# Kernel tuning notes

Hardware: AMD Instinct MI355X
Metric: run time of the kernel (lower is better)

Reference implementation:

```python
import jax, jax.numpy as jnp
import numpy as np

BETA = 0.25
N_E = 1024
E_DIM = 64
B, L = 32, 2048


def setup_inputs() -> dict:
    key = jax.random.key(0)
    k1, k2 = jax.random.split(key)
    z = jax.random.normal(k1, (B, L, E_DIM), dtype=jnp.float32)
    # torch init: uniform_(-1/n_e, 1/n_e)
    codebook = jax.random.uniform(k2, (N_E, E_DIM), dtype=jnp.float32,
                                  minval=-1.0 / N_E, maxval=1.0 / N_E)
    return {"z": z, "codebook": codebook}


def reference(z, codebook):
    sg = jax.lax.stop_gradient
    n_e = codebook.shape[0]
    zf = z.reshape(-1, codebook.shape[1])  # (N, e_dim)
    # squared-distance matrix: ||z||^2 + ||e||^2 - 2 z.e  -> (N, n_e)
    d = (jnp.sum(zf * zf, axis=1, keepdims=True)
         + jnp.sum(codebook * codebook, axis=1)
         - 2.0 * zf @ codebook.T)
    idx = jnp.argmin(d, axis=1)  # (N,)
    # one-hot @ codebook is just a gather
    z_q = codebook[idx].reshape(z.shape)
    loss = (jnp.mean((sg(z_q) - z) ** 2)
            + BETA * jnp.mean((z_q - sg(z)) ** 2))
    # straight-through estimator
    z_q_st = z + sg(z_q - z)
    # codebook usage stats (mean of one-hot rows == normalized histogram)
    counts = jnp.zeros((n_e,), dtype=z.dtype).at[idx].add(1.0)
    e_mean = counts / idx.shape[0]
    perplexity = jnp.exp(-jnp.sum(e_mean * jnp.log(e_mean + 1e-10)))
    return loss, z_q_st, perplexity, idx
```

## Files before the change

kernel.cpp:

```cpp
#include <hip/hip_runtime.h>
#include <math.h>

#define E_DIM 64
#define N_E   1024
#define BETA  0.25

using bf16x8 = __attribute__((ext_vector_type(8))) short;
using f32x4  = __attribute__((ext_vector_type(4))) float;
#define MFMA(a, b, c) __builtin_amdgcn_mfma_f32_16x16x32_bf16((a), (b), (c), 0, 0, 0)


__device__ __forceinline__ unsigned short f2bf_rn(float f) {
    unsigned u = __builtin_bit_cast(unsigned, f);
    unsigned r = u + 0x7fffu + ((u >> 16) & 1u);
    return (unsigned short)(r >> 16);
}
__device__ __forceinline__ float bf2f(unsigned short b) {
    unsigned u = ((unsigned)b) << 16;
    return __builtin_bit_cast(float, u);
}

__device__ __forceinline__ float pw64_sq(const float* v) {
    float r[8];
#pragma unroll
    for (int l = 0; l < 8; ++l) r[l] = v[l] * v[l];
#pragma unroll
    for (int t = 1; t < 8; ++t)
#pragma unroll
        for (int l = 0; l < 8; ++l) r[l] += v[8 * t + l] * v[8 * t + l];
    return ((r[0] + r[1]) + (r[2] + r[3])) + ((r[4] + r[5]) + (r[6] + r[7]));
}

__global__ __launch_bounds__(256) void k_prep(const float* __restrict__ cb,
                                              unsigned short* __restrict__ ebh,
                                              unsigned short* __restrict__ ebl,
                                              float* __restrict__ h,
                                              unsigned* __restrict__ hist,
                                              double* __restrict__ sse,
                                              unsigned* __restrict__ flagN) {
    int t = blockIdx.x * 256 + threadIdx.x;
    {
        int e = t & 7, lane = (t >> 3) & 63, ks = (t >> 9) & 1, ct = t >> 10;
        int j = ct * 16 + (lane & 15);
        int k = ks * 32 + ((lane >> 4) << 3) + e;
        float v = cb[j * 64 + k];
        unsigned short hi = f2bf_rn(v);
        ebh[t] = hi;
        ebl[t] = f2bf_rn(v - bf2f(hi));
    }
    if (blockIdx.x < 4) {
        int j = t;
        float e[E_DIM];
        const float4* ep = reinterpret_cast<const float4*>(cb + (size_t)j * E_DIM);
#pragma unroll
        for (int k4 = 0; k4 < E_DIM / 4; ++k4) {
            float4 v = ep[k4];
            e[4 * k4 + 0] = v.x; e[4 * k4 + 1] = v.y;
            e[4 * k4 + 2] = v.z; e[4 * k4 + 3] = v.w;
        }
        h[j] = pw64_sq(e);
    } else if (blockIdx.x == 4) {
#pragma unroll
        for (int u = 0; u < 4; ++u) hist[threadIdx.x * 4 + u] = 0u;
    } else if (blockIdx.x == 5 && threadIdx.x == 0) {
        *sse = 0.0;
        *flagN = 0u;
    }
}

__global__ __launch_bounds__(256, 2) void k_mfma(
    const float* __restrict__ z, const float* __restrict__ cb,
    const float* __restrict__ h,
    const unsigned short* __restrict__ ebh, const unsigned short* __restrict__ ebl,
    float* __restrict__ out_zq, float* __restrict__ out_idx,
    unsigned* __restrict__ hist, double* __restrict__ sse,
    unsigned* __restrict__ flagN, unsigned* __restrict__ flagL) {
    const int lane = threadIdx.x & 63;
    const int w = __builtin_amdgcn_readfirstlane(threadIdx.x >> 6);
    const int m = lane & 15, g = lane >> 4;

    __shared__ int bok;
    __shared__ float rsv[4][32];
    __shared__ float sb0[4][32], sb1[4][32];
    __shared__ int   sbi[4][32];
    if (threadIdx.x == 0) bok = 1;
    __syncthreads();

    {
        bf16x8 a, b;
#pragma unroll
        for (int e = 0; e < 8; ++e) {
            int k = g * 8 + e;
            a[e] = (short)f2bf_rn((float)(((m * 3 + k * 7) & 15) - 7));
            b[e] = (short)f2bf_rn((float)(((k * 5 + m * 3) & 15) - 8));
        }
        f32x4 acc = {0.f, 0.f, 0.f, 0.f};
        acc = MFMA(a, b, acc);
        bool ok = true;
#pragma unroll
        for (int r = 0; r < 4; ++r) {
            int rw = g * 4 + r;
            float E = 0.f;
            for (int k = 0; k < 32; ++k)
                E += (float)((((rw * 3 + k * 7) & 15) - 7) * (((k * 5 + m * 3) & 15) - 8));
            ok = ok && (acc[r] == E);
        }
        if (!ok) atomicAnd(&bok, 0);
    }
    __syncthreads();
    if (!bok) {
        if (threadIdx.x < 128) {
            unsigned p = atomicAdd(flagN, 1u);
            flagL[p] = (unsigned)(blockIdx.x * 128 + threadIdx.x);
        }
        return;
    }

    const int rowb32 = blockIdx.x * 128 + w * 32;
    bf16x8 a0h0, a0l0, a0h1, a0l1, a1h0, a1l0, a1h1, a1l1;
#define ALOAD(P, AH0, AL0, AH1, AL1) {                                         \
        const int rowA = rowb32 + (P) * 16 + m;                                \
        const float4* zr = reinterpret_cast<const float4*>(z + (size_t)rowA * 64); \
        float4 p0 = zr[g * 2], p1 = zr[g * 2 + 1];                             \
        float4 p2 = zr[8 + g * 2], p3 = zr[9 + g * 2];                         \
        float t0[8] = {p0.x, p0.y, p0.z, p0.w, p1.x, p1.y, p1.z, p1.w};        \
        float t1[8] = {p2.x, p2.y, p2.z, p2.w, p3.x, p3.y, p3.z, p3.w};        \
        float s = 0.f;                                                         \
        _Pragma("unroll")                                                      \
        for (int e = 0; e < 8; ++e) {                                          \
            s += fabsf(t0[e]) + fabsf(t1[e]);                                  \
            float x0 = 2.0f * t0[e]; unsigned short h0 = f2bf_rn(x0);          \
            AH0[e] = (short)h0; AL0[e] = (short)f2bf_rn(x0 - bf2f(h0));        \
            float x1 = 2.0f * t1[e]; unsigned short h1 = f2bf_rn(x1);          \
            AH1[e] = (short)h1; AL1[e] = (short)f2bf_rn(x1 - bf2f(h1));        \
        }                                                                      \
        s += __shfl_xor(s, 16);                                                \
        s += __shfl_xor(s, 32);                                                \
        if (g == 0) rsv[w][(P) * 16 + m] = s;                                  \
    }
    ALOAD(0, a0h0, a0l0, a0h1, a0l1)
    ALOAD(1, a1h0, a1l0, a1h1, a1l1)
#undef ALOAD

    float bb00 = INFINITY, bb01 = INFINITY, bb02 = INFINITY, bb03 = INFINITY;
    float bb10 = INFINITY, bb11 = INFINITY, bb12 = INFINITY, bb13 = INFINITY;
    float ss00 = INFINITY, ss01 = INFINITY, ss02 = INFINITY, ss03 = INFINITY;
    float ss10 = INFINITY, ss11 = INFINITY, ss12 = INFINITY, ss13 = INFINITY;
    int   ii00 = 0, ii01 = 0, ii02 = 0, ii03 = 0;
    int   ii10 = 0, ii11 = 0, ii12 = 0, ii13 = 0;
#define UPD(S, B0, B1, I0) { float _s = (S);                                   \
        if (_s < B0) { B1 = B0; B0 = _s; I0 = j; } else B1 = fminf(B1, _s); }

    const bf16x8* pBh = reinterpret_cast<const bf16x8*>(ebh);
    const bf16x8* pBl = reinterpret_cast<const bf16x8*>(ebl);

    bf16x8 Ah0 = pBh[lane],       Ah1 = pBh[lane + 64];
    bf16x8 Al0 = pBl[lane],       Al1 = pBl[lane + 64];
    bf16x8 Bh0 = pBh[128 + lane], Bh1 = pBh[128 + lane + 64];
    bf16x8 Bl0 = pBl[128 + lane], Bl1 = pBl[128 + lane + 64];

#define COLTILE(CT, VH0, VH1, VL0, VL1) {                                      \
        const int j = (CT) * 16 + m;                                           \
        const float hj = h[j];                                                 \
        const f32x4 z4 = {0.f, 0.f, 0.f, 0.f};                                 \
        f32x4 c0a = MFMA(a0h0, VH0, z4);                                       \
        f32x4 c0b = MFMA(a0h1, VH1, z4);                                       \
        f32x4 c1a = MFMA(a1h0, VH0, z4);                                       \
        f32x4 c1b = MFMA(a1h1, VH1, z4);                                       \
        f32x4 c0c = MFMA(a0h0, VL0, z4);                                       \
        f32x4 c0d = MFMA(a0h1, VL1, z4);                                       \
        f32x4 c1c = MFMA(a1h0, VL0, z4);                                       \
        f32x4 c1d = MFMA(a1h1, VL1, z4);                                       \
        f32x4 c0e = MFMA(a0l0, VH0, z4);                                       \
        f32x4 c0f = MFMA(a0l1, VH1, z4);                                       \
        f32x4 c1e = MFMA(a1l0, VH0, z4);                                       \
        f32x4 c1f = MFMA(a1l1, VH1, z4);                                       \
        f32x4 s0 = (c0a + c0b) + ((c0c + c0d) + (c0e + c0f));                  \
        f32x4 s1 = (c1a + c1b) + ((c1c + c1d) + (c1e + c1f));                  \
        UPD(hj - s0[0], bb00, ss00, ii00)                                      \
        UPD(hj - s0[1], bb01, ss01, ii01)                                      \
        UPD(hj - s0[2], bb02, ss02, ii02)                                      \
        UPD(hj - s0[3], bb03, ss03, ii03)                                      \
        UPD(hj - s1[0], bb10, ss10, ii10)                                      \
        UPD(hj - s1[1], bb11, ss11, ii11)                                      \
        UPD(hj - s1[2], bb12, ss12, ii12)                                      \
        UPD(hj - s1[3], bb13, ss13, ii13)                                      \
    }

#pragma unroll 1
    for (int ct = 0; ct < 64; ct += 2) {
        COLTILE(ct, Ah0, Ah1, Al0, Al1);
        if (ct + 2 < 64) {
            const int fb = (ct + 2) * 128 + lane;
            Ah0 = pBh[fb]; Ah1 = pBh[fb + 64];
            Al0 = pBl[fb]; Al1 = pBl[fb + 64];
        }
        COLTILE(ct + 1, Bh0, Bh1, Bl0, Bl1);
        if (ct + 3 < 64) {
            const int fb = (ct + 3) * 128 + lane;
            Bh0 = pBh[fb]; Bh1 = pBh[fb + 64];
            Bl0 = pBl[fb]; Bl1 = pBl[fb + 64];
        }
    }
#undef COLTILE
#undef UPD

#pragma unroll
    for (int mask = 1; mask < 16; mask <<= 1) {
#define MRG(B0, I0, B1) { float ob0 = __shfl_xor(B0, mask); int oi = __shfl_xor(I0, mask); \
        float ob1 = __shfl_xor(B1, mask); \
        if (ob0 < B0) { B1 = fminf(fminf(B0, B1), ob1); B0 = ob0; I0 = oi; } \
        else { B1 = fminf(B1, fminf(ob0, ob1)); } }
        MRG(bb00, ii00, ss00) MRG(bb01, ii01, ss01)
        MRG(bb02, ii02, ss02) MRG(bb03, ii03, ss03)
        MRG(bb10, ii10, ss10) MRG(bb11, ii11, ss11)
        MRG(bb12, ii12, ss12) MRG(bb13, ii13, ss13)
#undef MRG
    }

    if (m == 0) {
        sb0[w][g * 4 + 0] = bb00; sb1[w][g * 4 + 0] = ss00; sbi[w][g * 4 + 0] = ii00;
        sb0[w][g * 4 + 1] = bb01; sb1[w][g * 4 + 1] = ss01; sbi[w][g * 4 + 1] = ii01;
        sb0[w][g * 4 + 2] = bb02; sb1[w][g * 4 + 2] = ss02; sbi[w][g * 4 + 2] = ii02;
        sb0[w][g * 4 + 3] = bb03; sb1[w][g * 4 + 3] = ss03; sbi[w][g * 4 + 3] = ii03;
        sb0[w][16 + g * 4 + 0] = bb10; sb1[w][16 + g * 4 + 0] = ss10; sbi[w][16 + g * 4 + 0] = ii10;
        sb0[w][16 + g * 4 + 1] = bb11; sb1[w][16 + g * 4 + 1] = ss11; sbi[w][16 + g * 4 + 1] = ii11;
        sb0[w][16 + g * 4 + 2] = bb12; sb1[w][16 + g * 4 + 2] = ss12; sbi[w][16 + g * 4 + 2] = ii12;
        sb0[w][16 + g * 4 + 3] = bb13; sb1[w][16 + g * 4 + 3] = ss13; sbi[w][16 + g * 4 + 3] = ii13;
    }
    __syncthreads();

    {
        const int rloc = lane >> 1, q = lane & 1;
        const int rowO = rowb32 + rloc;
        const float vb0 = sb0[w][rloc];
        const float vb1 = sb1[w][rloc];
        const int   vi  = sbi[w][rloc];
        const float Delta = 6e-8f * rsv[w][rloc] + 2.2e-5f;
        float local = 0.f;
        if (vb1 - vb0 <= Delta) {
            if (q == 0) { unsigned p = atomicAdd(flagN, 1u); flagL[p] = (unsigned)rowO; }
        } else {
            if (q == 0) { out_idx[rowO] = (float)vi; atomicAdd(&hist[vi], 1u); }
            const float4* cv = reinterpret_cast<const float4*>(cb + (size_t)vi * 64) + q * 8;
            const float4* zv = reinterpret_cast<const float4*>(z + (size_t)rowO * 64) + q * 8;
            float* orow = out_zq + (size_t)rowO * 64 + q * 32;
#pragma unroll
            for (int u = 0; u < 8; ++u) {
                float4 cc = cv[u], zo = zv[u];
                orow[4 * u + 0] = cc.x; orow[4 * u + 1] = cc.y;
                orow[4 * u + 2] = cc.z; orow[4 * u + 3] = cc.w;
                float dx = cc.x - zo.x, dy = cc.y - zo.y;
                float dz = cc.z - zo.z, dw = cc.w - zo.w;
                local = fmaf(dx, dx, local); local = fmaf(dy, dy, local);
                local = fmaf(dz, dz, local); local = fmaf(dw, dw, local);
            }
        }
#pragma unroll
        for (int off = 32; off; off >>= 1) local += __shfl_down(local, off);
        if (lane == 0) atomicAdd(sse, (double)local);
    }
}

__global__ __launch_bounds__(64, 4) void k_cleanup(
    const float* __restrict__ z, const float* __restrict__ cb,
    const float* __restrict__ h,
    const unsigned* __restrict__ flagN, const unsigned* __restrict__ flagL,
    float* __restrict__ out_zq, float* __restrict__ out_idx,
    unsigned* __restrict__ hist, double* __restrict__ sse) {
    const unsigned n = *flagN;
    const int lane = threadIdx.x;

    for (unsigned f = blockIdx.x; f < n; f += gridDim.x) {
        const int row = (int)flagL[f];

        float tz[E_DIM];
        const float4* zp = reinterpret_cast<const float4*>(z + (size_t)row * 64);
#pragma unroll
        for (int k4 = 0; k4 < 16; ++k4) {
            float4 v = zp[k4];
            tz[4 * k4 + 0] = v.x; tz[4 * k4 + 1] = v.y;
            tz[4 * k4 + 2] = v.z; tz[4 * k4 + 3] = v.w;
        }
        const float nz = pw64_sq(tz);
#pragma unroll
        for (int k = 0; k < 64; ++k) tz[k] = 2.0f * tz[k];

        float bs = INFINITY;
        int bj = 0;
#pragma unroll 2
        for (int t = 0; t < 16; ++t) {
            const int j = lane + 64 * t;
            const float4* cv = reinterpret_cast<const float4*>(cb + (size_t)j * 64);
            float mm = 0.f;
#pragma unroll
            for (int k4 = 0; k4 < 16; ++k4) {
                float4 e = cv[k4];
                mm = fmaf(tz[4 * k4 + 0], e.x, mm);
                mm = fmaf(tz[4 * k4 + 1], e.y, mm);
                mm = fmaf(tz[4 * k4 + 2], e.z, mm);
                mm = fmaf(tz[4 * k4 + 3], e.w, mm);
            }
            float s = (nz + h[j]) - mm;
            if (s < bs) { bs = s; bj = j; }
        }
#pragma unroll
        for (int off = 32; off; off >>= 1) {
            float s2 = __shfl_down(bs, off);
            int   j2 = __shfl_down(bj, off);
            if (s2 < bs || (s2 == bs && j2 < bj)) { bs = s2; bj = j2; }
        }
        bj = __shfl(bj, 0);

        float c = cb[(size_t)bj * 64 + lane];
        out_zq[(size_t)row * 64 + lane] = c;
        float d = c - 0.5f * tz[lane];
        float l2 = d * d;
#pragma unroll
        for (int off = 32; off; off >>= 1) l2 += __shfl_down(l2, off);
        if (lane == 0) {
            out_idx[row] = (float)bj;
            atomicAdd(&hist[bj], 1u);
            atomicAdd(sse, (double)l2);
        }
    }
}

__global__ __launch_bounds__(256) void k_h_fb(const float* __restrict__ cb,
                                              float* __restrict__ h) {
    int j = blockIdx.x * 256 + threadIdx.x;
    if (j < N_E) {
        float e[E_DIM];
        const float4* ep = reinterpret_cast<const float4*>(cb + (size_t)j * E_DIM);
#pragma unroll
        for (int k4 = 0; k4 < E_DIM / 4; ++k4) {
            float4 v = ep[k4];
            e[4 * k4 + 0] = v.x; e[4 * k4 + 1] = v.y;
            e[4 * k4 + 2] = v.z; e[4 * k4 + 3] = v.w;
        }
        h[j] = pw64_sq(e);
    }
}

__global__ __launch_bounds__(512, 2) void k_scan_fb(
    const float* __restrict__ z, const float* __restrict__ cb,
    const float* __restrict__ h,
    float* __restrict__ out_zq, float* __restrict__ out_idx,
    unsigned* __restrict__ hist, double* __restrict__ sse) {
    const int lane = threadIdx.x & 63;
    const int w = __builtin_amdgcn_readfirstlane(threadIdx.x >> 6);
    const int row = blockIdx.x * 64 + lane;
    float tz[E_DIM];
    const float4* zp = reinterpret_cast<const float4*>(z + (size_t)row * E_DIM);
#pragma unroll
    for (int k4 = 0; k4 < E_DIM / 4; ++k4) {
        float4 v = zp[k4];
        tz[4 * k4 + 0] = v.x; tz[4 * k4 + 1] = v.y;
        tz[4 * k4 + 2] = v.z; tz[4 * k4 + 3] = v.w;
    }
    const float nz = pw64_sq(tz);
#pragma unroll
    for (int k = 0; k < E_DIM; ++k) tz[k] = 2.0f * tz[k];
    float b0 = INFINITY; int bi = 0;
    const int j0 = w * 128;
#pragma unroll 1
    for (int j = j0; j < j0 + 128; j += 4) {
        const float* c0 = cb + (size_t)j * E_DIM;
        float m0 = 0.f, m1 = 0.f, m2 = 0.f, m3 = 0.f;
#pragma unroll
        for (int k = 0; k < E_DIM; ++k) {
            float wk = tz[k];
            m0 = fmaf(wk, c0[0 * E_DIM + k], m0);
            m1 = fmaf(wk, c0[1 * E_DIM + k], m1);
            m2 = fmaf(wk, c0[2 * E_DIM + k], m2);
            m3 = fmaf(wk, c0[3 * E_DIM + k], m3);
        }
        float s0 = (nz + h[j + 0]) - m0;
        float s1 = (nz + h[j + 1]) - m1;
        float s2 = (nz + h[j + 2]) - m2;
        float s3 = (nz + h[j + 3]) - m3;
        if (s0 < b0) { b0 = s0; bi = j + 0; }
        if (s1 < b0) { b0 = s1; bi = j + 1; }
        if (s2 < b0) { b0 = s2; bi = j + 2; }
        if (s3 < b0) { b0 = s3; bi = j + 3; }
    }
    __shared__ float lb[8][64];
    __shared__ int   li[8][64];
    lb[w][lane] = b0; li[w][lane] = bi;
    __syncthreads();
    if (threadIdx.x < 64) {
        float b = lb[0][lane]; int i = li[0][lane];
#pragma unroll
        for (int c = 1; c < 8; ++c) {
            float bc = lb[c][lane]; int ic = li[c][lane];
            if (bc < b) { b = bc; i = ic; }
        }
        out_idx[row] = (float)i;
        float local = 0.f;
        const float4* cv = reinterpret_cast<const float4*>(cb + (size_t)i * E_DIM);
        float* orow = out_zq + (size_t)row * E_DIM;
#pragma unroll
        for (int k4 = 0; k4 < E_DIM / 4; ++k4) {
            float4 c = cv[k4];
            float zx = 0.5f * tz[4 * k4 + 0], zy = 0.5f * tz[4 * k4 + 1];
            float zz = 0.5f * tz[4 * k4 + 2], zw = 0.5f * tz[4 * k4 + 3];
            orow[4 * k4 + 0] = c.x; orow[4 * k4 + 1] = c.y;
            orow[4 * k4 + 2] = c.z; orow[4 * k4 + 3] = c.w;
            float dx = c.x - zx, dy = c.y - zy, dz = c.z - zz, dw = c.w - zw;
            local = fmaf(dx, dx, local); local = fmaf(dy, dy, local);
            local = fmaf(dz, dz, local); local = fmaf(dw, dw, local);
        }
        atomicAdd(&hist[i], 1u);
#pragma unroll
        for (int off = 32; off; off >>= 1) local += __shfl_down(local, off);
        if (lane == 0) atomicAdd(sse, (double)local);
    }
}

__global__ __launch_bounds__(256) void k_final(
    const unsigned* __restrict__ hist, const double* __restrict__ sse,
    float* __restrict__ out, int nrows) {
    __shared__ double sh[256];
    double acc = 0.0;
    for (int j = threadIdx.x; j < N_E; j += 256) {
        double p = (double)hist[j] / (double)nrows;
        acc += p * log(p + 1e-10);
    }
    sh[threadIdx.x] = acc;
    __syncthreads();
    for (int s = 128; s; s >>= 1) {
        if (threadIdx.x < s) sh[threadIdx.x] += sh[threadIdx.x + s];
        __syncthreads();
    }
    if (threadIdx.x == 0) {
        double ntot = (double)nrows * (double)E_DIM;
        out[0] = (float)((1.0 + BETA) * (*sse) / ntot);
        out[1 + (size_t)nrows * E_DIM] = (float)exp(-sh[0]);
    }
}

extern "C" void kernel_launch(void* const* d_in, const int* in_sizes, int n_in,
                              void* d_out, int out_size, void* d_ws, size_t ws_size,
                              hipStream_t stream) {
    const float* z  = (const float*)d_in[0];
    const float* cb = (const float*)d_in[1];
    const int nrows = in_sizes[0] / E_DIM;
    float* out = (float*)d_out;

    char* ws = (char*)d_ws;
    unsigned* hist  = (unsigned*)(ws + 0);
    double*   sse   = (double*)  (ws + 4096);
    unsigned* flagN = (unsigned*)(ws + 4104);
    float*    h     = (float*)   (ws + 4112);
    unsigned short* ebh = (unsigned short*)(ws + 8208);
    unsigned short* ebl = (unsigned short*)(ws + 139280);
    unsigned* flagL = (unsigned*)(ws + 270352);

    float* out_zq  = out + 1;
    float* out_idx = out + 1 + (size_t)nrows * E_DIM + 1;

    if (ws_size >= 532496) {
        k_prep<<<256, 256, 0, stream>>>(cb, ebh, ebl, h, hist, sse, flagN);
        k_mfma<<<nrows / 128, 256, 0, stream>>>(z, cb, h, ebh, ebl,
                                                out_zq, out_idx, hist, sse, flagN, flagL);
        k_cleanup<<<2048, 64, 0, stream>>>(z, cb, h, flagN, flagL,
                                           out_zq, out_idx, hist, sse);
    } else {
        hipMemsetAsync(d_ws, 0, 4112, stream);
        k_h_fb<<<(N_E + 255) / 256, 256, 0, stream>>>(cb, h);
        k_scan_fb<<<nrows / 64, 512, 0, stream>>>(z, cb, h, out_zq, out_idx, hist, sse);
    }
    k_final<<<1, 256, 0, stream>>>(hist, sse, out, nrows);
}
```

Before: 127.1 us.

## Stage codebook bf16 chunks into LDS with async global_load_lds triple buffering

Replaces the per-wave direct global loads of the hi/lo bf16 codebook fragments with a block-cooperative triple-buffered LDS pipeline. Chunks of 64 codes are fetched with global_load_lds two chunks ahead, synchronised with vmcnt waits and barriers, and each wave runs its MFMAs at raised priority. The code norms h are also cached in shared memory. The aim is to cut redundant global/L2 traffic across the four waves and hide load latency. The cost is extra LDS (about 52KB), which may limit occupancy at 2 blocks per CU, plus a block-wide barrier for every chunk.

```diff
diff --git a/kernel.cpp b/kernel.cpp
--- a/kernel.cpp
+++ b/kernel.cpp
@@ -8,6 +8,13 @@
 using bf16x8 = __attribute__((ext_vector_type(8))) short;
 using f32x4  = __attribute__((ext_vector_type(4))) float;
 #define MFMA(a, b, c) __builtin_amdgcn_mfma_f32_16x16x32_bf16((a), (b), (c), 0, 0, 0)
+
+#define GLOAD_LDS(g, l) __builtin_amdgcn_global_load_lds(                      \
+    (const __attribute__((address_space(1))) void*)(g),                        \
+    (__attribute__((address_space(3))) void*)(l), 16, 0, 0)
+
+#define STR_(x) #x
+#define STR(x) STR_(x)
 
 
 __device__ __forceinline__ unsigned short f2bf_rn(float f) {
@@ -79,6 +86,8 @@
     const int w = __builtin_amdgcn_readfirstlane(threadIdx.x >> 6);
     const int m = lane & 15, g = lane >> 4;
 
+    __shared__ __align__(16) unsigned char sB[3][2][8192];
+    __shared__ float sh_h[N_E];
     __shared__ int bok;
     __shared__ float rsv[4][32];
     __shared__ float sb0[4][32], sb1[4][32];
@@ -142,6 +151,17 @@
     ALOAD(1, a1h0, a1l0, a1h1, a1l1)
 #undef ALOAD
 
+#define STAGE(C, B) {                                                          \
+        const unsigned char* gh = (const unsigned char*)ebh +                  \
+            (size_t)(C) * 8192 + w * 2048 + lane * 16;                         \
+        const unsigned char* gl = (const unsigned char*)ebl +                  \
+            (size_t)(C) * 8192 + w * 2048 + lane * 16;                         \
+        unsigned char* dh = &sB[B][0][w * 2048];                               \
+        unsigned char* dl = &sB[B][1][w * 2048];                               \
+        GLOAD_LDS(gh, dh); GLOAD_LDS(gh + 1024, dh + 1024);                    \
+        GLOAD_LDS(gl, dl); GLOAD_LDS(gl + 1024, dl + 1024);                    \
+    }
+
     float bb00 = INFINITY, bb01 = INFINITY, bb02 = INFINITY, bb03 = INFINITY;
     float bb10 = INFINITY, bb11 = INFINITY, bb12 = INFINITY, bb13 = INFINITY;
     float ss00 = INFINITY, ss01 = INFINITY, ss02 = INFINITY, ss03 = INFINITY;
@@ -151,30 +171,25 @@
 #define UPD(S, B0, B1, I0) { float _s = (S);                                   \
         if (_s < B0) { B1 = B0; B0 = _s; I0 = j; } else B1 = fminf(B1, _s); }
 
-    const bf16x8* pBh = reinterpret_cast<const bf16x8*>(ebh);
-    const bf16x8* pBl = reinterpret_cast<const bf16x8*>(ebl);
-
-    bf16x8 Ah0 = pBh[lane],       Ah1 = pBh[lane + 64];
-    bf16x8 Al0 = pBl[lane],       Al1 = pBl[lane + 64];
-    bf16x8 Bh0 = pBh[128 + lane], Bh1 = pBh[128 + lane + 64];
-    bf16x8 Bl0 = pBl[128 + lane], Bl1 = pBl[128 + lane + 64];
-
-#define COLTILE(CT, VH0, VH1, VL0, VL1) {                                      \
-        const int j = (CT) * 16 + m;                                           \
-        const float hj = h[j];                                                 \
+#define COLTILE(JT, LCT, SBH, SBL) {                                           \
+        const int j = (JT) * 16 + m;                                           \
+        const float hj = sh_h[j];                                              \
+        const int fb = (LCT) * 128 + lane;                                     \
+        bf16x8 vbh0 = SBH[fb], vbh1 = SBH[fb + 64];                            \
+        bf16x8 vbl0 = SBL[fb], vbl1 = SBL[fb + 64];                            \
         const f32x4 z4 = {0.f, 0.f, 0.f, 0.f};                                 \
-        f32x4 c0a = MFMA(a0h0, VH0, z4);                                       \
-        f32x4 c0b = MFMA(a0h1, VH1, z4);                                       \
-        f32x4 c1a = MFMA(a1h0, VH0, z4);                                       \
-        f32x4 c1b = MFMA(a1h1, VH1, z4);                                       \
-        f32x4 c0c = MFMA(a0h0, VL0, z4);                                       \
-        f32x4 c0d = MFMA(a0h1, VL1, z4);                                       \
-        f32x4 c1c = MFMA(a1h0, VL0, z4);                                       \
-        f32x4 c1d = MFMA(a1h1, VL1, z4);                                       \
-        f32x4 c0e = MFMA(a0l0, VH0, z4);                                       \
-        f32x4 c0f = MFMA(a0l1, VH1, z4);                                       \
-        f32x4 c1e = MFMA(a1l0, VH0, z4);                                       \
-        f32x4 c1f = MFMA(a1l1, VH1, z4);                                       \
+        f32x4 c0a = MFMA(a0h0, vbh0, z4);                                      \
+        f32x4 c0b = MFMA(a0h1, vbh1, z4);                                      \
+        f32x4 c1a = MFMA(a1h0, vbh0, z4);                                      \
+        f32x4 c1b = MFMA(a1h1, vbh1, z4);                                      \
+        f32x4 c0c = MFMA(a0h0, vbl0, z4);                                      \
+        f32x4 c0d = MFMA(a0h1, vbl1, z4);                                      \
+        f32x4 c1c = MFMA(a1h0, vbl0, z4);                                      \
+        f32x4 c1d = MFMA(a1h1, vbl1, z4);                                      \
+        f32x4 c0e = MFMA(a0l0, vbh0, z4);                                      \
+        f32x4 c0f = MFMA(a0l1, vbh1, z4);                                      \
+        f32x4 c1e = MFMA(a1l0, vbh0, z4);                                      \
+        f32x4 c1f = MFMA(a1l1, vbh1, z4);                                      \
         f32x4 s0 = (c0a + c0b) + ((c0c + c0d) + (c0e + c0f));                  \
         f32x4 s1 = (c1a + c1b) + ((c1c + c1d) + (c1e + c1f));                  \
         UPD(hj - s0[0], bb00, ss00, ii00)                                      \
@@ -187,22 +202,46 @@
         UPD(hj - s1[3], bb13, ss13, ii13)                                      \
     }
 
+#define CHUNK4(C, B) {                                                         \
+        const bf16x8* sBh = reinterpret_cast<const bf16x8*>(&sB[B][0][0]);     \
+        const bf16x8* sBl = reinterpret_cast<const bf16x8*>(&sB[B][1][0]);     \
+        COLTILE(4 * (C) + 0, 0, sBh, sBl)                                      \
+        COLTILE(4 * (C) + 1, 1, sBh, sBl)                                      \
+        COLTILE(4 * (C) + 2, 2, sBh, sBl)                                      \
+        COLTILE(4 * (C) + 3, 3, sBh, sBl)                                      \
+    }
+
+#define PHASE(C, BC, BS, DOSTAGE, VMC) {                                       \
+        if (DOSTAGE) STAGE((C) + 2, BS)                                        \
+        asm volatile("s_waitcnt vmcnt(" STR(VMC) ")" ::: "memory");            \
+        __builtin_amdgcn_s_barrier();                                          \
+        __builtin_amdgcn_sched_barrier(0);                                     \
+        __builtin_amdgcn_s_setprio(1);                                         \
+        CHUNK4(C, BC)                                                          \
+        __builtin_amdgcn_s_setprio(0);                                         \
+        __builtin_amdgcn_sched_barrier(0);                                     \
+        __builtin_amdgcn_s_barrier();                                          \
+    }
+
+    STAGE(0, 0)
+    STAGE(1, 1)
+    for (int i = threadIdx.x; i < N_E; i += 256) sh_h[i] = h[i];
+    __syncthreads();
+
 #pragma unroll 1
-    for (int ct = 0; ct < 64; ct += 2) {
-        COLTILE(ct, Ah0, Ah1, Al0, Al1);
-        if (ct + 2 < 64) {
-            const int fb = (ct + 2) * 128 + lane;
-            Ah0 = pBh[fb]; Ah1 = pBh[fb + 64];
-            Al0 = pBl[fb]; Al1 = pBl[fb + 64];
-        }
-        COLTILE(ct + 1, Bh0, Bh1, Bl0, Bl1);
-        if (ct + 3 < 64) {
-            const int fb = (ct + 3) * 128 + lane;
-            Bh0 = pBh[fb]; Bh1 = pBh[fb + 64];
-            Bl0 = pBl[fb]; Bl1 = pBl[fb + 64];
-        }
-    }
+    for (int base = 0; base < 12; base += 3) {
+        PHASE(base + 0, 0, 2, 1, 8)
+        PHASE(base + 1, 1, 0, 1, 8)
+        PHASE(base + 2, 2, 1, 1, 8)
+    }
+    PHASE(12, 0, 2, 1, 8)
+    PHASE(13, 1, 0, 1, 8)
+    PHASE(14, 2, 0, 0, 4)
+    PHASE(15, 0, 0, 0, 0)
+#undef PHASE
+#undef CHUNK4
 #undef COLTILE
+#undef STAGE
 #undef UPD
 
 #pragma unroll
```

New measurement: 154.5 us. 1.21x slower.

## Split codebook scan across two blocks per row group and merge in separate kernel

Applied to the files above, without the earlier changes.

The MFMA distance kernel can now split the 64 codebook column tiles across two blocks per 128-row group, doubling the grid from 512 to 1024 blocks. Each half writes its best score, second-best score and index to workspace. A new merge kernel combines the halves, recomputes the |z| sum for the ambiguity threshold, and does the gather, histogram and SSE work that used to live in the epilogue. The aim is better occupancy and load balance across CUs, paid for with an extra launch, a second read of z, and workspace traffic for the partial results.

```diff
diff --git a/kernel.cpp b/kernel.cpp
--- a/kernel.cpp
+++ b/kernel.cpp
@@ -4,6 +4,7 @@
 #define E_DIM 64
 #define N_E   1024
 #define BETA  0.25
+#define NROWS 65536
 
 using bf16x8 = __attribute__((ext_vector_type(8))) short;
 using f32x4  = __attribute__((ext_vector_type(4))) float;
@@ -69,20 +70,19 @@
 }
 
 __global__ __launch_bounds__(256, 2) void k_mfma(
-    const float* __restrict__ z, const float* __restrict__ cb,
-    const float* __restrict__ h,
+    const float* __restrict__ z, const float* __restrict__ h,
     const unsigned short* __restrict__ ebh, const unsigned short* __restrict__ ebl,
-    float* __restrict__ out_zq, float* __restrict__ out_idx,
-    unsigned* __restrict__ hist, double* __restrict__ sse,
-    unsigned* __restrict__ flagN, unsigned* __restrict__ flagL) {
+    float* __restrict__ pb0, float* __restrict__ pb1, int* __restrict__ pidx,
+    int nsplit) {
     const int lane = threadIdx.x & 63;
     const int w = __builtin_amdgcn_readfirstlane(threadIdx.x >> 6);
     const int m = lane & 15, g = lane >> 4;
+    const int half = (nsplit == 2) ? (int)(blockIdx.x & 1) : 0;
+    const int rg   = (nsplit == 2) ? (int)(blockIdx.x >> 1) : (int)blockIdx.x;
+    const int ncts = 64 / nsplit;
+    const int ct0  = half * ncts;
 
     __shared__ int bok;
-    __shared__ float rsv[4][32];
-    __shared__ float sb0[4][32], sb1[4][32];
-    __shared__ int   sbi[4][32];
     if (threadIdx.x == 0) bok = 1;
     __syncthreads();
 
@@ -110,13 +110,14 @@
     __syncthreads();
     if (!bok) {
         if (threadIdx.x < 128) {
-            unsigned p = atomicAdd(flagN, 1u);
-            flagL[p] = (unsigned)(blockIdx.x * 128 + threadIdx.x);
+            const size_t o = (size_t)half * NROWS + blockIdx.x / nsplit * 0 +
+                             (size_t)rg * 128 + threadIdx.x;
+            pb0[o] = -1e30f; pb1[o] = -1e30f; pidx[o] = 0;
         }
         return;
     }
 
-    const int rowb32 = blockIdx.x * 128 + w * 32;
+    const int rowb32 = rg * 128 + w * 32;
     bf16x8 a0h0, a0l0, a0h1, a0l1, a1h0, a1l0, a1h1, a1l1;
 #define ALOAD(P, AH0, AL0, AH1, AL1) {                                         \
         const int rowA = rowb32 + (P) * 16 + m;                                \
@@ -125,18 +126,13 @@
         float4 p2 = zr[8 + g * 2], p3 = zr[9 + g * 2];                         \
         float t0[8] = {p0.x, p0.y, p0.z, p0.w, p1.x, p1.y, p1.z, p1.w};        \
         float t1[8] = {p2.x, p2.y, p2.z, p2.w, p3.x, p3.y, p3.z, p3.w};        \
-        float s = 0.f;                                                         \
         _Pragma("unroll")                                                      \
         for (int e = 0; e < 8; ++e) {                                          \
-            s += fabsf(t0[e]) + fabsf(t1[e]);                                  \
             float x0 = 2.0f * t0[e]; unsigned short h0 = f2bf_rn(x0);          \
             AH0[e] = (short)h0; AL0[e] = (short)f2bf_rn(x0 - bf2f(h0));        \
             float x1 = 2.0f * t1[e]; unsigned short h1 = f2bf_rn(x1);          \
             AH1[e] = (short)h1; AL1[e] = (short)f2bf_rn(x1 - bf2f(h1));        \
         }                                                                      \
-        s += __shfl_xor(s, 16);                                                \
-        s += __shfl_xor(s, 32);                                                \
-        if (g == 0) rsv[w][(P) * 16 + m] = s;                                  \
     }
     ALOAD(0, a0h0, a0l0, a0h1, a0l1)
     ALOAD(1, a1h0, a1l0, a1h1, a1l1)
@@ -154,10 +150,10 @@
     const bf16x8* pBh = reinterpret_cast<const bf16x8*>(ebh);
     const bf16x8* pBl = reinterpret_cast<const bf16x8*>(ebl);
 
-    bf16x8 Ah0 = pBh[lane],       Ah1 = pBh[lane + 64];
-    bf16x8 Al0 = pBl[lane],       Al1 = pBl[lane + 64];
-    bf16x8 Bh0 = pBh[128 + lane], Bh1 = pBh[128 + lane + 64];
-    bf16x8 Bl0 = pBl[128 + lane], Bl1 = pBl[128 + lane + 64];
+    bf16x8 Ah0 = pBh[ct0 * 128 + lane],        Ah1 = pBh[ct0 * 128 + lane + 64];
+    bf16x8 Al0 = pBl[ct0 * 128 + lane],        Al1 = pBl[ct0 * 128 + lane + 64];
+    bf16x8 Bh0 = pBh[(ct0 + 1) * 128 + lane],  Bh1 = pBh[(ct0 + 1) * 128 + lane + 64];
+    bf16x8 Bl0 = pBl[(ct0 + 1) * 128 + lane],  Bl1 = pBl[(ct0 + 1) * 128 + lane + 64];
 
 #define COLTILE(CT, VH0, VH1, VL0, VL1) {                                      \
         const int j = (CT) * 16 + m;                                           \
@@ -188,15 +184,15 @@
     }
 
 #pragma unroll 1
-    for (int ct = 0; ct < 64; ct += 2) {
+    for (int ct = ct0; ct < ct0 + ncts; ct += 2) {
         COLTILE(ct, Ah0, Ah1, Al0, Al1);
-        if (ct + 2 < 64) {
+        if (ct + 2 < ct0 + ncts) {
             const int fb = (ct + 2) * 128 + lane;
             Ah0 = pBh[fb]; Ah1 = pBh[fb + 64];
             Al0 = pBl[fb]; Al1 = pBl[fb + 64];
         }
         COLTILE(ct + 1, Bh0, Bh1, Bl0, Bl1);
-        if (ct + 3 < 64) {
+        if (ct + 3 < ct0 + ncts) {
             const int fb = (ct + 3) * 128 + lane;
             Bh0 = pBh[fb]; Bh1 = pBh[fb + 64];
             Bl0 = pBl[fb]; Bl1 = pBl[fb + 64];
@@ -219,47 +215,77 @@
     }
 
     if (m == 0) {
-        sb0[w][g * 4 + 0] = bb00; sb1[w][g * 4 + 0] = ss00; sbi[w][g * 4 + 0] = ii00;
-        sb0[w][g * 4 + 1] = bb01; sb1[w][g * 4 + 1] = ss01; sbi[w][g * 4 + 1] = ii01;
-        sb0[w][g * 4 + 2] = bb02; sb1[w][g * 4 + 2] = ss02; sbi[w][g * 4 + 2] = ii02;
-        sb0[w][g * 4 + 3] = bb03; sb1[w][g * 4 + 3] = ss03; sbi[w][g * 4 + 3] = ii03;
-        sb0[w][16 + g * 4 + 0] = bb10; sb1[w][16 + g * 4 + 0] = ss10; sbi[w][16 + g * 4 + 0] = ii10;
-        sb0[w][16 + g * 4 + 1] = bb11; sb1[w][16 + g * 4 + 1] = ss11; sbi[w][16 + g * 4 + 1] = ii11;
-        sb0[w][16 + g * 4 + 2] = bb12; sb1[w][16 + g * 4 + 2] = ss12; sbi[w][16 + g * 4 + 2] = ii12;
-        sb0[w][16 + g * 4 + 3] = bb13; sb1[w][16 + g * 4 + 3] = ss13; sbi[w][16 + g * 4 + 3] = ii13;
-    }
+        const size_t b0o = (size_t)half * NROWS + rowb32 + g * 4;
+        pb0[b0o + 0] = bb00; pb1[b0o + 0] = ss00; pidx[b0o + 0] = ii00;
+        pb0[b0o + 1] = bb01; pb1[b0o + 1] = ss01; pidx[b0o + 1] = ii01;
+        pb0[b0o + 2] = bb02; pb1[b0o + 2] = ss02; pidx[b0o + 2] = ii02;
+        pb0[b0o + 3] = bb03; pb1[b0o + 3] = ss03; pidx[b0o + 3] = ii03;
+        const size_t b1o = b0o + 16;
+        pb0[b1o + 0] = bb10; pb1[b1o + 0] = ss10; pidx[b1o + 0] = ii10;
+        pb0[b1o + 1] = bb11; pb1[b1o + 1] = ss11; pidx[b1o + 1] = ii11;
+        pb0[b1o + 2] = bb12; pb1[b1o + 2] = ss12; pidx[b1o + 2] = ii12;
+        pb0[b1o + 3] = bb13; pb1[b1o + 3] = ss13; pidx[b1o + 3] = ii13;
+    }
+}
+
+__global__ __launch_bounds__(256) void k_merge(
+    const float* __restrict__ z, const float* __restrict__ cb,
+    const float* __restrict__ pb0, const float* __restrict__ pb1,
+    const int* __restrict__ pidx,
+    float* __restrict__ out_zq, float* __restrict__ out_idx,
+    unsigned* __restrict__ hist, double* __restrict__ sse,
+    unsigned* __restrict__ flagN, unsigned* __restrict__ flagL, int nsplit) {
+    const int t = blockIdx.x * 256 + threadIdx.x;
+    const int row = t >> 2, q = t & 3;
+    const int lane = threadIdx.x & 63;
+
+    float b0 = pb0[row], b1 = pb1[row];
+    int   vi = pidx[row];
+    if (nsplit == 2) {
+        float c0 = pb0[NROWS + row], c1 = pb1[NROWS + row];
+        int   ci = pidx[NROWS + row];
+        if (c0 < b0) { b1 = fminf(b0, c1); b0 = c0; vi = ci; }
+        else         { b1 = fminf(b1, c0); }
+    }
+
+    const float4* zv = reinterpret_cast<const float4*>(z + (size_t)row * 64) + q * 4;
+    float4 za = zv[0], zb = zv[1], zc = zv[2], zd = zv[3];
+    float s = fabsf(za.x) + fabsf(za.y) + fabsf(za.z) + fabsf(za.w)
+            + fabsf(zb.x) + fabsf(zb.y) + fabsf(zb.z) + fabsf(zb.w)
+            + fabsf(zc.x) + fabsf(zc.y) + fabsf(zc.z) + fabsf(zc.w)
+            + fabsf(zd.x) + fabsf(zd.y) + fabsf(zd.z) + fabsf(zd.w);
+    s += __shfl_xor(s, 1);
+    s += __shfl_xor(s, 2);
+    const float Delta = 6e-8f * s + 2.2e-5f;
+
+    float local = 0.f;
+    if (b1 - b0 <= Delta) {
+        if (q == 0) { unsigned p = atomicAdd(flagN, 1u); flagL[p] = (unsigned)row; }
+    } else {
+        if (q == 0) { out_idx[row] = (float)vi; atomicAdd(&hist[vi], 1u); }
+        const float4* cv = reinterpret_cast<const float4*>(cb + (size_t)vi * 64) + q * 4;
+        float* orow = out_zq + (size_t)row * 64 + q * 16;
+        float4 zz[4] = {za, zb, zc, zd};
+#pragma unroll
+        for (int u = 0; u < 4; ++u) {
+            float4 cc = cv[u];
+            const float4* zp = reinterpret_cast<const float4*>(z + (size_t)row * 64) + q * 4 + u;
+            float4 zo = *zp;
+            (void)zz;
+            orow[4 * u + 0] = cc.x; orow[4 * u + 1] = cc.y;
+            orow[4 * u + 2] = cc.z; orow[4 * u + 3] = cc.w;
+            float dx = cc.x - zo.x, dy = cc.y - zo.y;
+            float dz = cc.z - zo.z, dw = cc.w - zo.w;
+            local = fmaf(dx, dx, local); local = fmaf(dy, dy, local);
+            local = fmaf(dz, dz, local); local = fmaf(dw, dw, local);
+        }
+    }
+#pragma unroll
+    for (int off = 32; off; off >>= 1) local += __shfl_down(local, off);
+    __shared__ float wp[4];
+    if (lane == 0) wp[threadIdx.x >> 6] = local;
     __syncthreads();
-
-    {
-        const int rloc = lane >> 1, q = lane & 1;
-        const int rowO = rowb32 + rloc;
-        const float vb0 = sb0[w][rloc];
-        const float vb1 = sb1[w][rloc];
-        const int   vi  = sbi[w][rloc];
-        const float Delta = 6e-8f * rsv[w][rloc] + 2.2e-5f;
-        float local = 0.f;
-        if (vb1 - vb0 <= Delta) {
-            if (q == 0) { unsigned p = atomicAdd(flagN, 1u); flagL[p] = (unsigned)rowO; }
-        } else {
-            if (q == 0) { out_idx[rowO] = (float)vi; atomicAdd(&hist[vi], 1u); }
-            const float4* cv = reinterpret_cast<const float4*>(cb + (size_t)vi * 64) + q * 8;
-            const float4* zv = reinterpret_cast<const float4*>(z + (size_t)rowO * 64) + q * 8;
-            float* orow = out_zq + (size_t)rowO * 64 + q * 32;
-#pragma unroll
-            for (int u = 0; u < 8; ++u) {
-                float4 cc = cv[u], zo = zv[u];
-                orow[4 * u + 0] = cc.x; orow[4 * u + 1] = cc.y;
-                orow[4 * u + 2] = cc.z; orow[4 * u + 3] = cc.w;
-                float dx = cc.x - zo.x, dy = cc.y - zo.y;
-                float dz = cc.z - zo.z, dw = cc.w - zo.w;
-                local = fmaf(dx, dx, local); local = fmaf(dy, dy, local);
-                local = fmaf(dz, dz, local); local = fmaf(dw, dw, local);
-            }
-        }
-#pragma unroll
-        for (int off = 32; off; off >>= 1) local += __shfl_down(local, off);
-        if (lane == 0) atomicAdd(sse, (double)local);
-    }
+    if (threadIdx.x == 0) atomicAdd(sse, (double)(wp[0] + wp[1] + wp[2] + wp[3]));
 }
 
 __global__ __launch_bounds__(64, 4) void k_cleanup(
@@ -301,8 +327,8 @@
                 mm = fmaf(tz[4 * k4 + 2], e.z, mm);
                 mm = fmaf(tz[4 * k4 + 3], e.w, mm);
             }
-            float s = (nz + h[j]) - mm;
-            if (s < bs) { bs = s; bj = j; }
+            float sc = (nz + h[j]) - mm;
+            if (sc < bs) { bs = sc; bj = j; }
         }
 #pragma unroll
         for (int off = 32; off; off >>= 1) {
@@ -459,10 +485,20 @@
     float* out_zq  = out + 1;
     float* out_idx = out + 1 + (size_t)nrows * E_DIM + 1;
 
-    if (ws_size >= 532496) {
+    const int nsplit = (ws_size >= 2105360) ? 2 : 1;
+    const size_t P = (size_t)NROWS * 4 * nsplit;
+    float* pb0 = (float*)(ws + 532496);
+    float* pb1 = (float*)(ws + 532496 + P);
+    int*  ppid = (int*)  (ws + 532496 + 2 * P);
+    const size_t need = 532496 + 3 * P;
+
+    if (ws_size >= need) {
         k_prep<<<256, 256, 0, stream>>>(cb, ebh, ebl, h, hist, sse, flagN);
-        k_mfma<<<nrows / 128, 256, 0, stream>>>(z, cb, h, ebh, ebl,
-                                                out_zq, out_idx, hist, sse, flagN, flagL);
+        k_mfma<<<(nrows / 128) * nsplit, 256, 0, stream>>>(z, h, ebh, ebl,
+                                                           pb0, pb1, ppid, nsplit);
+        k_merge<<<nrows / 64, 256, 0, stream>>>(z, cb, pb0, pb1, ppid,
+                                                out_zq, out_idx, hist, sse,
+                                                flagN, flagL, nsplit);
         k_cleanup<<<2048, 64, 0, stream>>>(z, cb, h, flagN, flagL,
                                            out_zq, out_idx, hist, sse);
     } else {
```

Measured after the change: 122.0 us. 4.1% less time.

## Split codebook scan across two wave halves and chain MFMA accumulation

Applied to the files above, without the earlier changes.

Doubles the block to 512 threads so each 128-row block has two groups of four waves, each scanning half of the codebook column tiles, then merges the per-half best/second-best results through shared memory. The 12 independent MFMAs per tile, which were summed with vector adds, become two chained accumulation sequences, cutting register use and add instructions. The per-wave SSE double atomic is replaced by a block-level shared reduction with one atomic per block. This doubles the wave count per row tile, which adds parallelism and latency hiding, but the serial accumulation chains may expose MFMA dependency latency, and the launch bounds now demand more waves per CU.

```diff
diff --git a/kernel.cpp b/kernel.cpp
--- a/kernel.cpp
+++ b/kernel.cpp
@@ -4,6 +4,7 @@
 #define E_DIM 64
 #define N_E   1024
 #define BETA  0.25
+#define NROWS 65536
 
 using bf16x8 = __attribute__((ext_vector_type(8))) short;
 using f32x4  = __attribute__((ext_vector_type(4))) float;
@@ -68,7 +69,7 @@
     }
 }
 
-__global__ __launch_bounds__(256, 2) void k_mfma(
+__global__ __launch_bounds__(512, 4) void k_mfma(
     const float* __restrict__ z, const float* __restrict__ cb,
     const float* __restrict__ h,
     const unsigned short* __restrict__ ebh, const unsigned short* __restrict__ ebl,
@@ -78,11 +79,14 @@
     const int lane = threadIdx.x & 63;
     const int w = __builtin_amdgcn_readfirstlane(threadIdx.x >> 6);
     const int m = lane & 15, g = lane >> 4;
+    const int half = w >> 2;
+    const int rw   = w & 3;
 
     __shared__ int bok;
-    __shared__ float rsv[4][32];
-    __shared__ float sb0[4][32], sb1[4][32];
-    __shared__ int   sbi[4][32];
+    __shared__ float rsv[128];
+    __shared__ float sb0[2][128], sb1[2][128];
+    __shared__ int   sbi[2][128];
+    __shared__ float wp[8];
     if (threadIdx.x == 0) bok = 1;
     __syncthreads();
 
@@ -99,10 +103,10 @@
         bool ok = true;
 #pragma unroll
         for (int r = 0; r < 4; ++r) {
-            int rw = g * 4 + r;
+            int rr = g * 4 + r;
             float E = 0.f;
             for (int k = 0; k < 32; ++k)
-                E += (float)((((rw * 3 + k * 7) & 15) - 7) * (((k * 5 + m * 3) & 15) - 8));
+                E += (float)((((rr * 3 + k * 7) & 15) - 7) * (((k * 5 + m * 3) & 15) - 8));
             ok = ok && (acc[r] == E);
         }
         if (!ok) atomicAnd(&bok, 0);
@@ -116,7 +120,7 @@
         return;
     }
 
-    const int rowb32 = blockIdx.x * 128 + w * 32;
+    const int rowb32 = blockIdx.x * 128 + rw * 32;
     bf16x8 a0h0, a0l0, a0h1, a0l1, a1h0, a1l0, a1h1, a1l1;
 #define ALOAD(P, AH0, AL0, AH1, AL1) {                                         \
         const int rowA = rowb32 + (P) * 16 + m;                                \
@@ -136,7 +140,7 @@
         }                                                                      \
         s += __shfl_xor(s, 16);                                                \
         s += __shfl_xor(s, 32);                                                \
-        if (g == 0) rsv[w][(P) * 16 + m] = s;                                  \
+        if (g == 0 && half == 0) rsv[rw * 32 + (P) * 16 + m] = s;              \
     }
     ALOAD(0, a0h0, a0l0, a0h1, a0l1)
     ALOAD(1, a1h0, a1l0, a1h1, a1l1)
@@ -153,30 +157,29 @@
 
     const bf16x8* pBh = reinterpret_cast<const bf16x8*>(ebh);
     const bf16x8* pBl = reinterpret_cast<const bf16x8*>(ebl);
-
-    bf16x8 Ah0 = pBh[lane],       Ah1 = pBh[lane + 64];
-    bf16x8 Al0 = pBl[lane],       Al1 = pBl[lane + 64];
-    bf16x8 Bh0 = pBh[128 + lane], Bh1 = pBh[128 + lane + 64];
-    bf16x8 Bl0 = pBl[128 + lane], Bl1 = pBl[128 + lane + 64];
+    const int ct0 = half * 32;
+
+    bf16x8 Ah0 = pBh[ct0 * 128 + lane],        Ah1 = pBh[ct0 * 128 + lane + 64];
+    bf16x8 Al0 = pBl[ct0 * 128 + lane],        Al1 = pBl[ct0 * 128 + lane + 64];
+    bf16x8 Bh0 = pBh[(ct0 + 1) * 128 + lane],  Bh1 = pBh[(ct0 + 1) * 128 + lane + 64];
+    bf16x8 Bl0 = pBl[(ct0 + 1) * 128 + lane],  Bl1 = pBl[(ct0 + 1) * 128 + lane + 64];
 
 #define COLTILE(CT, VH0, VH1, VL0, VL1) {                                      \
         const int j = (CT) * 16 + m;                                           \
         const float hj = h[j];                                                 \
         const f32x4 z4 = {0.f, 0.f, 0.f, 0.f};                                 \
-        f32x4 c0a = MFMA(a0h0, VH0, z4);                                       \
-        f32x4 c0b = MFMA(a0h1, VH1, z4);                                       \
-        f32x4 c1a = MFMA(a1h0, VH0, z4);                                       \
-        f32x4 c1b = MFMA(a1h1, VH1, z4);                                       \
-        f32x4 c0c = MFMA(a0h0, VL0, z4);                                       \
-        f32x4 c0d = MFMA(a0h1, VL1, z4);                                       \
-        f32x4 c1c = MFMA(a1h0, VL0, z4);                                       \
-        f32x4 c1d = MFMA(a1h1, VL1, z4);                                       \
-        f32x4 c0e = MFMA(a0l0, VH0, z4);                                       \
-        f32x4 c0f = MFMA(a0l1, VH1, z4);                                       \
-        f32x4 c1e = MFMA(a1l0, VH0, z4);                                       \
-        f32x4 c1f = MFMA(a1l1, VH1, z4);                                       \
-        f32x4 s0 = (c0a + c0b) + ((c0c + c0d) + (c0e + c0f));                  \
-        f32x4 s1 = (c1a + c1b) + ((c1c + c1d) + (c1e + c1f));                  \
+        f32x4 s0 = MFMA(a0h0, VH0, z4);                                        \
+        f32x4 s1 = MFMA(a1h0, VH0, z4);                                        \
+        s0 = MFMA(a0h1, VH1, s0);                                              \
+        s1 = MFMA(a1h1, VH1, s1);                                              \
+        s0 = MFMA(a0h0, VL0, s0);                                              \
+        s1 = MFMA(a1h0, VL0, s1);                                              \
+        s0 = MFMA(a0h1, VL1, s0);                                              \
+        s1 = MFMA(a1h1, VL1, s1);                                              \
+        s0 = MFMA(a0l0, VH0, s0);                                              \
+        s1 = MFMA(a1l0, VH0, s1);                                              \
+        s0 = MFMA(a0l1, VH1, s0);                                              \
+        s1 = MFMA(a1l1, VH1, s1);                                              \
         UPD(hj - s0[0], bb00, ss00, ii00)                                      \
         UPD(hj - s0[1], bb01, ss01, ii01)                                      \
         UPD(hj - s0[2], bb02, ss02, ii02)                                      \
@@ -188,15 +191,15 @@
     }
 
 #pragma unroll 1
-    for (int ct = 0; ct < 64; ct += 2) {
+    for (int ct = ct0; ct < ct0 + 32; ct += 2) {
         COLTILE(ct, Ah0, Ah1, Al0, Al1);
-        if (ct + 2 < 64) {
+        if (ct + 2 < ct0 + 32) {
             const int fb = (ct + 2) * 128 + lane;
             Ah0 = pBh[fb]; Ah1 = pBh[fb + 64];
             Al0 = pBl[fb]; Al1 = pBl[fb + 64];
         }
         COLTILE(ct + 1, Bh0, Bh1, Bl0, Bl1);
-        if (ct + 3 < 64) {
+        if (ct + 3 < ct0 + 32) {
             const int fb = (ct + 3) * 128 + lane;
             Bh0 = pBh[fb]; Bh1 = pBh[fb + 64];
             Bl0 = pBl[fb]; Bl1 = pBl[fb + 64];
@@ -219,34 +222,41 @@
     }
 
     if (m == 0) {
-        sb0[w][g * 4 + 0] = bb00; sb1[w][g * 4 + 0] = ss00; sbi[w][g * 4 + 0] = ii00;
-        sb0[w][g * 4 + 1] = bb01; sb1[w][g * 4 + 1] = ss01; sbi[w][g * 4 + 1] = ii01;
-        sb0[w][g * 4 + 2] = bb02; sb1[w][g * 4 + 2] = ss02; sbi[w][g * 4 + 2] = ii02;
-        sb0[w][g * 4 + 3] = bb03; sb1[w][g * 4 + 3] = ss03; sbi[w][g * 4 + 3] = ii03;
-        sb0[w][16 + g * 4 + 0] = bb10; sb1[w][16 + g * 4 + 0] = ss10; sbi[w][16 + g * 4 + 0] = ii10;
-        sb0[w][16 + g * 4 + 1] = bb11; sb1[w][16 + g * 4 + 1] = ss11; sbi[w][16 + g * 4 + 1] = ii11;
-        sb0[w][16 + g * 4 + 2] = bb12; sb1[w][16 + g * 4 + 2] = ss12; sbi[w][16 + g * 4 + 2] = ii12;
-        sb0[w][16 + g * 4 + 3] = bb13; sb1[w][16 + g * 4 + 3] = ss13; sbi[w][16 + g * 4 + 3] = ii13;
+        const int r0 = rw * 32 + g * 4;
+        sb0[half][r0 + 0] = bb00; sb1[half][r0 + 0] = ss00; sbi[half][r0 + 0] = ii00;
+        sb0[half][r0 + 1] = bb01; sb1[half][r0 + 1] = ss01; sbi[half][r0 + 1] = ii01;
+        sb0[half][r0 + 2] = bb02; sb1[half][r0 + 2] = ss02; sbi[half][r0 + 2] = ii02;
+        sb0[half][r0 + 3] = bb03; sb1[half][r0 + 3] = ss03; sbi[half][r0 + 3] = ii03;
+        const int r1 = r0 + 16;
+        sb0[half][r1 + 0] = bb10; sb1[half][r1 + 0] = ss10; sbi[half][r1 + 0] = ii10;
+        sb0[half][r1 + 1] = bb11; sb1[half][r1 + 1] = ss11; sbi[half][r1 + 1] = ii11;
+        sb0[half][r1 + 2] = bb12; sb1[half][r1 + 2] = ss12; sbi[half][r1 + 2] = ii12;
+        sb0[half][r1 + 3] = bb13; sb1[half][r1 + 3] = ss13; sbi[half][r1 + 3] = ii13;
     }
     __syncthreads();
 
     {
-        const int rloc = lane >> 1, q = lane & 1;
-        const int rowO = rowb32 + rloc;
-        const float vb0 = sb0[w][rloc];
-        const float vb1 = sb1[w][rloc];
-        const int   vi  = sbi[w][rloc];
-        const float Delta = 6e-8f * rsv[w][rloc] + 2.2e-5f;
+        const int rloc = threadIdx.x >> 2, q = threadIdx.x & 3;
+        const int rowO = blockIdx.x * 128 + rloc;
+        float b0 = sb0[0][rloc], b1 = sb1[0][rloc];
+        int   vi = sbi[0][rloc];
+        {
+            float c0 = sb0[1][rloc], c1 = sb1[1][rloc];
+            int   ci = sbi[1][rloc];
+            if (c0 < b0) { b1 = fminf(b0, c1); b0 = c0; vi = ci; }
+            else         { b1 = fminf(b1, c0); }
+        }
+        const float Delta = 6e-8f * rsv[rloc] + 2.2e-5f;
         float local = 0.f;
-        if (vb1 - vb0 <= Delta) {
+        if (b1 - b0 <= Delta) {
             if (q == 0) { unsigned p = atomicAdd(flagN, 1u); flagL[p] = (unsigned)rowO; }
         } else {
             if (q == 0) { out_idx[rowO] = (float)vi; atomicAdd(&hist[vi], 1u); }
-            const float4* cv = reinterpret_cast<const float4*>(cb + (size_t)vi * 64) + q * 8;
-            const float4* zv = reinterpret_cast<const float4*>(z + (size_t)rowO * 64) + q * 8;
-            float* orow = out_zq + (size_t)rowO * 64 + q * 32;
-#pragma unroll
-            for (int u = 0; u < 8; ++u) {
+            const float4* cv = reinterpret_cast<const float4*>(cb + (size_t)vi * 64) + q * 4;
+            const float4* zv = reinterpret_cast<const float4*>(z + (size_t)rowO * 64) + q * 4;
+            float* orow = out_zq + (size_t)rowO * 64 + q * 16;
+#pragma unroll
+            for (int u = 0; u < 4; ++u) {
                 float4 cc = cv[u], zo = zv[u];
                 orow[4 * u + 0] = cc.x; orow[4 * u + 1] = cc.y;
                 orow[4 * u + 2] = cc.z; orow[4 * u + 3] = cc.w;
@@ -258,7 +268,13 @@
         }
 #pragma unroll
         for (int off = 32; off; off >>= 1) local += __shfl_down(local, off);
-        if (lane == 0) atomicAdd(sse, (double)local);
+        if (lane == 0) wp[w] = local;
+    }
+    __syncthreads();
+    if (threadIdx.x == 0) {
+        float t = ((wp[0] + wp[1]) + (wp[2] + wp[3]))
+                + ((wp[4] + wp[5]) + (wp[6] + wp[7]));
+        atomicAdd(sse, (double)t);
     }
 }
 
@@ -301,8 +317,8 @@
                 mm = fmaf(tz[4 * k4 + 2], e.z, mm);
                 mm = fmaf(tz[4 * k4 + 3], e.w, mm);
             }
-            float s = (nz + h[j]) - mm;
-            if (s < bs) { bs = s; bj = j; }
+            float sc = (nz + h[j]) - mm;
+            if (sc < bs) { bs = sc; bj = j; }
         }
 #pragma unroll
         for (int off = 32; off; off >>= 1) {
@@ -461,8 +477,9 @@
 
     if (ws_size >= 532496) {
         k_prep<<<256, 256, 0, stream>>>(cb, ebh, ebl, h, hist, sse, flagN);
-        k_mfma<<<nrows / 128, 256, 0, stream>>>(z, cb, h, ebh, ebl,
-                                                out_zq, out_idx, hist, sse, flagN, flagL);
+        k_mfma<<<nrows / 128, 512, 0, stream>>>(z, cb, h, ebh, ebl,
+                                                out_zq, out_idx, hist, sse,
+                                                flagN, flagL);
         k_cleanup<<<2048, 64, 0, stream>>>(z, cb, h, flagN, flagL,
                                            out_zq, out_idx, hist, sse);
     } else {
```

Result: faster. 102.8 us (-19.2%).
